# Optimization experiments

Measured on AMD Instinct MI355X. Metric: run time of the kernel, lower is better.

Reference implementation:

```python
import jax, jax.numpy as jnp
import numpy as np

B, S, E = 2, 2048, 1024
H, D = 16, 64  # num_heads, head_dim


def setup_inputs() -> dict:
    key = jax.random.key(0)
    k1, k2, k3 = jax.random.split(key, 3)
    x = jax.random.normal(k1, (B, S, E), dtype=jnp.float32)
    # nnx normal() init has stddev 0.01; scale to keep magnitudes realistic
    w_qkv = jax.random.normal(k2, (E, H, 3 * D), dtype=jnp.float32) * 0.01
    w_out = jax.random.normal(k3, (H, D, E), dtype=jnp.float32) * 0.01
    return {"x": x, "w_qkv": w_qkv, "w_out": w_out}


def _attention(q, k, v):
    # q,k,v: [B, S, H, D]
    dtype = q.dtype
    logits = jnp.einsum('bqhd,bkhd->bhqk', q.astype(jnp.float32), k.astype(jnp.float32))
    logits = logits / jnp.sqrt(jnp.float32(q.shape[-1]))
    mask = jnp.tril(jnp.ones((q.shape[1], q.shape[1]), dtype=jnp.bool_))
    neg = jnp.asarray(-0.7 * jnp.finfo(logits.dtype).max, dtype=logits.dtype)
    logits = jnp.where(mask, logits, neg)
    probs = jax.nn.softmax(logits, axis=-1).astype(dtype)
    return jnp.einsum('bhqk,bkhd->bqhd', probs, v)


def reference(x, w_qkv, w_out):
    # qkv projection: [B,S,E] x [E,H,3D] -> [B,S,H,3D]
    qkv = jnp.einsum('bse,ehd->bshd', x, w_qkv)
    q, k, v = jnp.split(qkv, 3, axis=-1)
    out = _attention(q, k, v)  # [B,S,H,D]
    # output projection contracts (H,D) -> E
    return jnp.einsum('bshd,hde->bse', out, w_out)
```

## Files before the change

kernel.cpp:

```cpp
#include <hip/hip_runtime.h>

typedef unsigned short u16;
typedef unsigned int u32;
typedef __attribute__((ext_vector_type(8))) short bf16x8;
typedef __attribute__((ext_vector_type(4))) float f32x4;
typedef __attribute__((ext_vector_type(16))) float f32x16;
typedef __attribute__((ext_vector_type(4))) u32 u32x4;

#define MFMA16(a, b, c) __builtin_amdgcn_mfma_f32_16x16x32_bf16((a), (b), (c), 0, 0, 0)
#define MFMA32(a, b, c) __builtin_amdgcn_mfma_f32_32x32x16_bf16((a), (b), (c), 0, 0, 0)

__device__ __forceinline__ void async_lds16(void* lds, const void* g) {
  __builtin_amdgcn_global_load_lds(
      (const __attribute__((address_space(1))) void*)g,
      (__attribute__((address_space(3))) void*)lds, 16, 0, 0);
}

__device__ __forceinline__ u16 f2bf(float f) {
  union { float f; unsigned u; } v; v.f = f;
  unsigned r = v.u + 0x7fffu + ((v.u >> 16) & 1u);
  return (u16)(r >> 16);
}

__device__ __forceinline__ u32 cvt_pk_bf16(float lo, float hi) {
  u32 r;
  asm("v_cvt_pk_bf16_f32 %0, %1, %2" : "=v"(r) : "v"(lo), "v"(hi));
  return r;
}

__device__ __forceinline__ float exp2_fast(float x) {
  float r;
  asm("v_exp_f32 %0, %1" : "=v"(r) : "v"(x));
  return r;
}

__device__ __forceinline__ void pswap(u32& a, u32& b) {
  asm("v_permlane32_swap_b32 %0, %1" : "+v"(a), "+v"(b));
}


__device__ __forceinline__ void transpose_cvt_body(const float* __restrict__ in, u16* __restrict__ out,
                                                   int R, int C, int bx, int by,
                                                   float (*tile)[33]) {
  int c0 = bx * 32, r0 = by * 32;
  int tx = threadIdx.x & 31, ty = threadIdx.x >> 5;
#pragma unroll
  for (int i = 0; i < 32; i += 8)
    tile[ty + i][tx] = in[(long)(r0 + ty + i) * C + c0 + tx];
  __syncthreads();
#pragma unroll
  for (int i = 0; i < 32; i += 8)
    out[(long)(c0 + ty + i) * R + r0 + tx] = f2bf(tile[tx][ty + i]);
}

__global__ __launch_bounds__(256) void k_prep(const float* __restrict__ x, u16* __restrict__ xb,
                                              const float* __restrict__ w_qkv, u16* __restrict__ wqkvT,
                                              const float* __restrict__ w_out, u16* __restrict__ woutT) {
  __shared__ float tile[32][33];
  const int B = blockIdx.x;
  if (B < 4096) {
    int i = (B * 256 + threadIdx.x) * 4;
    float4 v = *(const float4*)(x + i);
    ushort4 o;
    o.x = f2bf(v.x); o.y = f2bf(v.y); o.z = f2bf(v.z); o.w = f2bf(v.w);
    *(ushort4*)(xb + i) = o;
  } else if (B < 7168) {
    int bb = B - 4096;
    transpose_cvt_body(w_qkv, wqkvT, 1024, 3072, bb % 96, bb / 96, tile);
  } else {
    int bb = B - 7168;
    transpose_cvt_body(w_out, woutT, 1024, 1024, bb & 31, bb >> 5, tile);
  }
}

__global__ __launch_bounds__(256) void k_transpose_v(const u16* __restrict__ V, u16* __restrict__ Vt) {
  int bh = blockIdx.z;
  int s0 = blockIdx.x * 32, d0 = blockIdx.y * 32;
  __shared__ u16 tile[32][33];
  int tx = threadIdx.x & 31, ty = threadIdx.x >> 5;
  const u16* Vb = V + (long)bh * 2048 * 64;
  u16* Vtb = Vt + (long)bh * 64 * 2048;
#pragma unroll
  for (int i = 0; i < 32; i += 8)
    tile[ty + i][tx] = Vb[(long)(s0 + ty + i) * 64 + d0 + tx];
  __syncthreads();
#pragma unroll
  for (int i = 0; i < 32; i += 8)
    Vtb[(long)(d0 + ty + i) * 2048 + s0 + tx] = tile[tx][ty + i];
}


template <int BM, int BN, int NW, int WN, int WCS, int MR, int NR, int NLD>
__device__ __forceinline__ void gemm_core_pipe(const u16* __restrict__ A, const u16* __restrict__ Bt,
                                               int K, long row0, long col0,
                                               u16* sA, u16* sB, f32x4 (&acc)[MR][NR]) {
  const int NTHR = NW * 64;
  const int ABYTES = BM * 64 * 2;
  const int BBYTES = BN * 64 * 2;
  const int t = threadIdx.x;
  const int lane = t & 63, g = lane >> 4, m16 = lane & 15;
  const int wid = t >> 6, wr = wid / WN, wc = wid % WN;
  const int nkt = K >> 6;

  auto stage = [&](int buf, int kt) {
    const int k0 = kt << 6;
#pragma unroll
    for (int it = 0; it < ABYTES / (NTHR * 16); ++it) {
      int i = it * NTHR + t;
      int r = i >> 3, c = i & 7, cs = c ^ (r & 7);
      async_lds16((char*)sA + buf * ABYTES + i * 16, A + (row0 + r) * K + k0 + cs * 8);
    }
#pragma unroll
    for (int it = 0; it < BBYTES / (NTHR * 16); ++it) {
      int i = it * NTHR + t;
      int r = i >> 3, c = i & 7, cs = c ^ (r & 7);
      async_lds16((char*)sB + buf * BBYTES + i * 16, Bt + (col0 + r) * K + k0 + cs * 8);
    }
  };

  stage(0, 0);
  stage(1, 1);
  int cur = 0;
  for (int kt = 0; kt < nkt; ++kt) {
    if (kt + 1 < nkt) {
      if constexpr (NLD == 7) asm volatile("s_waitcnt vmcnt(7)" ::: "memory");
      else                    asm volatile("s_waitcnt vmcnt(8)" ::: "memory");
    } else {
      asm volatile("s_waitcnt vmcnt(0)" ::: "memory");
    }
    __builtin_amdgcn_s_barrier();
    __builtin_amdgcn_sched_barrier(0);
    const char* bA = (const char*)sA + cur * ABYTES;
    const char* bB = (const char*)sB + cur * BBYTES;
#pragma unroll
    for (int kk6 = 0; kk6 < 2; ++kk6) {
      const int ke = kk6 * 32 + 8 * g;
      bf16x8 av[MR], bv[NR];
#pragma unroll
      for (int mi = 0; mi < MR; ++mi) {
        int row = wr * (MR * 16) + mi * 16 + m16;
        av[mi] = *(const bf16x8*)(bA + (row << 7) + ((ke << 1) ^ ((row & 7) << 4)));
      }
#pragma unroll
      for (int ni = 0; ni < NR; ++ni) {
        int row = wc * WCS + ni * 16 + m16;
        bv[ni] = *(const bf16x8*)(bB + (row << 7) + ((ke << 1) ^ ((row & 7) << 4)));
      }
#pragma unroll
      for (int mi = 0; mi < MR; ++mi)
#pragma unroll
        for (int ni = 0; ni < NR; ++ni)
          acc[mi][ni] = MFMA16(av[mi], bv[ni], acc[mi][ni]);
    }
    __builtin_amdgcn_sched_barrier(0);
    __builtin_amdgcn_s_barrier();
    if (kt + 2 < nkt) stage(cur, kt + 2);
    cur ^= 1;
  }
}

__global__ __launch_bounds__(512, 2) void k_gemm_qkv(const u16* __restrict__ xb, const u16* __restrict__ wT,
                                                     u16* __restrict__ Qo, u16* __restrict__ Ko,
                                                     u16* __restrict__ Vo) {
  __shared__ __align__(16) u16 sA[2 * 256 * 64];
  __shared__ __align__(16) u16 sB[2 * 192 * 64];
  f32x4 acc[8][3];
  const f32x4 z = {0.f, 0.f, 0.f, 0.f};
#pragma unroll
  for (int mi = 0; mi < 8; ++mi)
#pragma unroll
    for (int ni = 0; ni < 3; ++ni) acc[mi][ni] = z;
  const int L = blockIdx.x;
  const int xcd = L & 7, idx = L >> 3;
  const int rowt = xcd * 2 + (idx & 1);
  const int colt = idx >> 1;
  long row0 = (long)rowt * 256, col0 = (long)colt * 192;
  gemm_core_pipe<256, 192, 8, 4, 48, 8, 3, 7>(xb, wT, 1024, row0, col0, sA, sB, acc);
  const int t = threadIdx.x;
  const int lane = t & 63, g = lane >> 4, m16 = lane & 15;
  const int wid = t >> 6, wr = wid >> 2, wc = wid & 3;
  const int h = colt;
#pragma unroll
  for (int mi = 0; mi < 8; ++mi) {
#pragma unroll
    for (int ni = 0; ni < 3; ++ni) {
      int rem = wc * 48 + ni * 16 + m16;
      int which = rem >> 6, d = rem & 63;
#pragma unroll
      for (int r = 0; r < 4; ++r) {
        int row = (int)row0 + wr * 128 + mi * 16 + 4 * g + r;
        int b = row >> 11, s = row & 2047;
        long off = (((long)(b * 16 + h)) * 2048 + s) * 64 + d;
        float v = acc[mi][ni][r];
        if (which == 0) Qo[off] = f2bf(v * 0.18033688f);
        else if (which == 1) Ko[off] = f2bf(v);
        else Vo[off] = f2bf(v);
      }
    }
  }
}

__global__ __launch_bounds__(256) void k_gemm_out(const u16* __restrict__ Ob, const u16* __restrict__ wT,
                                                  float* __restrict__ out) {
  __shared__ __align__(16) u16 sA[2 * 128 * 64];
  __shared__ __align__(16) u16 sB[2 * 128 * 64];
  f32x4 acc[4][4];
  const f32x4 z = {0.f, 0.f, 0.f, 0.f};
#pragma unroll
  for (int mi = 0; mi < 4; ++mi)
#pragma unroll
    for (int ni = 0; ni < 4; ++ni) acc[mi][ni] = z;
  const int L = blockIdx.x;
  const int xcd = L & 7, idx = L >> 3;
  const int rowt = xcd * 4 + (idx & 3);
  const int colt = idx >> 2;
  long row0 = (long)rowt * 128, col0 = (long)colt * 128;
  gemm_core_pipe<128, 128, 4, 2, 64, 4, 4, 8>(Ob, wT, 1024, row0, col0, sA, sB, acc);
  const int t = threadIdx.x;
  const int lane = t & 63, g = lane >> 4, m16 = lane & 15;
  const int wid = t >> 6, wr = wid >> 1, wc = wid & 1;
#pragma unroll
  for (int mi = 0; mi < 4; ++mi) {
#pragma unroll
    for (int ni = 0; ni < 4; ++ni) {
#pragma unroll
      for (int r = 0; r < 4; ++r) {
        long row = row0 + wr * 64 + mi * 16 + 4 * g + r;
        long col = col0 + wc * 64 + ni * 16 + m16;
        out[row * 1024 + col] = acc[mi][ni][r];
      }
    }
  }
}


template <bool DIAG>
__device__ __forceinline__ void attn_sub(const char* Kt, const char* Vt, int bsub,
                                         bf16x8 qf0, bf16x8 qf1, bf16x8 qf2, bf16x8 qf3,
                                         f32x16& acc0, f32x16& acc1, float& l,
                                         int q5, int hi) {
  const int x7 = q5 & 7;
  const int rowK = (bsub * 32 + q5) << 7;
  bf16x8 k0 = *(const bf16x8*)(Kt + rowK + (((0 + hi) ^ x7) << 4));
  bf16x8 k1 = *(const bf16x8*)(Kt + rowK + (((2 + hi) ^ x7) << 4));
  bf16x8 k2 = *(const bf16x8*)(Kt + rowK + (((4 + hi) ^ x7) << 4));
  bf16x8 k3 = *(const bf16x8*)(Kt + rowK + (((6 + hi) ^ x7) << 4));
  const int rowV0 = q5 << 7, rowV1 = (q5 + 32) << 7;
  bf16x8 v00 = *(const bf16x8*)(Vt + rowV0 + (((bsub * 4 + 0 + hi) ^ x7) << 4));
  bf16x8 v01 = *(const bf16x8*)(Vt + rowV1 + (((bsub * 4 + 0 + hi) ^ x7) << 4));
  bf16x8 v10 = *(const bf16x8*)(Vt + rowV0 + (((bsub * 4 + 2 + hi) ^ x7) << 4));
  bf16x8 v11 = *(const bf16x8*)(Vt + rowV1 + (((bsub * 4 + 2 + hi) ^ x7) << 4));

  f32x16 s;
#pragma unroll
  for (int r = 0; r < 16; ++r) s[r] = 0.f;
  __builtin_amdgcn_s_setprio(1);
  s = MFMA32(k0, qf0, s);
  s = MFMA32(k1, qf1, s);
  s = MFMA32(k2, qf2, s);
  s = MFMA32(k3, qf3, s);
  __builtin_amdgcn_s_setprio(0);

  float p[16];
#pragma unroll
  for (int r = 0; r < 16; ++r) {
    float pv = exp2_fast(s[r]);
    if (DIAG) {
      int crow = (r & 3) + 8 * (r >> 2) + 4 * hi;
      pv = (crow <= q5) ? pv : 0.f;
    }
    p[r] = pv;
  }
  l += (((p[0] + p[1]) + (p[2] + p[3])) + ((p[4] + p[5]) + (p[6] + p[7]))) +
       (((p[8] + p[9]) + (p[10] + p[11])) + ((p[12] + p[13]) + (p[14] + p[15])));

  u32 a0 = cvt_pk_bf16(p[0], p[1]), a1 = cvt_pk_bf16(p[2], p[3]);
  u32 b0 = cvt_pk_bf16(p[4], p[5]), b1 = cvt_pk_bf16(p[6], p[7]);
  pswap(a0, b0); pswap(a1, b1);
  u32 c0 = cvt_pk_bf16(p[8], p[9]), c1 = cvt_pk_bf16(p[10], p[11]);
  u32 d0 = cvt_pk_bf16(p[12], p[13]), d1 = cvt_pk_bf16(p[14], p[15]);
  pswap(c0, d0); pswap(c1, d1);
  u32x4 t0; t0[0] = a0; t0[1] = a1; t0[2] = b0; t0[3] = b1;
  u32x4 t1; t1[0] = c0; t1[1] = c1; t1[2] = d0; t1[3] = d1;
  bf16x8 pa0 = __builtin_bit_cast(bf16x8, t0);
  bf16x8 pa1 = __builtin_bit_cast(bf16x8, t1);

  __builtin_amdgcn_s_setprio(1);
  acc0 = MFMA32(pa0, v00, acc0);
  acc1 = MFMA32(pa0, v01, acc1);
  acc0 = MFMA32(pa1, v10, acc0);
  acc1 = MFMA32(pa1, v11, acc1);
  __builtin_amdgcn_s_setprio(0);
}

__global__ __launch_bounds__(256) void k_attn(const u16* __restrict__ Qg, const u16* __restrict__ Kg,
                                              const u16* __restrict__ Vtg, u16* __restrict__ Og) {
  __shared__ __align__(16) u16 sK[4][64 * 64];
  __shared__ __align__(16) u16 sV[4][64 * 64];
  const int t = threadIdx.x;
  const int lane = t & 63, q5 = lane & 31, hi = lane >> 5, w = t >> 6;
  const int L = blockIdx.x;
  const int bh = L & 31, pr = L >> 5;
  const int qtA = pr, qtB = 15 - pr;
  const int b = bh >> 4, h = bh & 15;
  const u16* Qh = Qg + (long)bh * 131072;
  const u16* Kh = Kg + (long)bh * 131072;
  const u16* Vh = Vtg + (long)bh * 131072;
  char* sKb = (char*)sK;
  char* sVb = (char*)sV;

  const int sL_ = qtA * 4 + w, sH_ = qtB * 4 + w;
  const int q0L = sL_ * 32, q0H = sH_ * 32;
  const int nkt = 2 * qtB + 2;

  const u16* QpL = Qh + (long)(q0L + q5) * 64 + hi * 8;
  bf16x8 qfL0 = *(const bf16x8*)(QpL);
  bf16x8 qfL1 = *(const bf16x8*)(QpL + 16);
  bf16x8 qfL2 = *(const bf16x8*)(QpL + 32);
  bf16x8 qfL3 = *(const bf16x8*)(QpL + 48);
  const u16* QpH = Qh + (long)(q0H + q5) * 64 + hi * 8;
  bf16x8 qfH0 = *(const bf16x8*)(QpH);
  bf16x8 qfH1 = *(const bf16x8*)(QpH + 16);
  bf16x8 qfH2 = *(const bf16x8*)(QpH + 32);
  bf16x8 qfH3 = *(const bf16x8*)(QpH + 48);

  f32x16 aL0, aL1, aH0, aH1;
#pragma unroll
  for (int r = 0; r < 16; ++r) { aL0[r] = 0.f; aL1[r] = 0.f; aH0[r] = 0.f; aH1[r] = 0.f; }
  float lL = 0.f, lH = 0.f;

  auto stage = [&](int buf, int kt) {
    const int kbase = kt << 6;
#pragma unroll
    for (int ps = 0; ps < 2; ++ps) {
      int i = ps * 256 + t;
      int r = i >> 3, c = i & 7, cs = c ^ (r & 7);
      async_lds16(sKb + buf * 8192 + i * 16, Kh + (long)(kbase + r) * 64 + cs * 8);
    }
#pragma unroll
    for (int ps = 0; ps < 2; ++ps) {
      int i = ps * 256 + t;
      int d = i >> 3, c = i & 7, cs = c ^ (d & 7);
      async_lds16(sVb + buf * 8192 + i * 16, Vh + (long)d * 2048 + kbase + cs * 8);
    }
  };

  stage(0, 0);
  stage(1, 1);
  stage(2, 2);
  stage(3, 3);
#pragma unroll 1
  for (int kt = 0; kt < nkt; ++kt) {
    const int rem = nkt - kt;
    if (rem > 3)       asm volatile("s_waitcnt vmcnt(12)" ::: "memory");
    else if (rem == 3) asm volatile("s_waitcnt vmcnt(8)" ::: "memory");
    else if (rem == 2) asm volatile("s_waitcnt vmcnt(4)" ::: "memory");
    else               asm volatile("s_waitcnt vmcnt(0)" ::: "memory");
    __builtin_amdgcn_s_barrier();
    __builtin_amdgcn_sched_barrier(0);
    const char* Kt = sKb + (kt & 3) * 8192;
    const char* Vt = sVb + (kt & 3) * 8192;
    const int c2 = 2 * kt;
    if (c2 <= sH_) {
      if (c2 == sH_) attn_sub<true>(Kt, Vt, 0, qfH0, qfH1, qfH2, qfH3, aH0, aH1, lH, q5, hi);
      else           attn_sub<false>(Kt, Vt, 0, qfH0, qfH1, qfH2, qfH3, aH0, aH1, lH, q5, hi);
    }
    if (c2 + 1 <= sH_) {
      if (c2 + 1 == sH_) attn_sub<true>(Kt, Vt, 1, qfH0, qfH1, qfH2, qfH3, aH0, aH1, lH, q5, hi);
      else               attn_sub<false>(Kt, Vt, 1, qfH0, qfH1, qfH2, qfH3, aH0, aH1, lH, q5, hi);
    }
    if (c2 <= sL_) {
      if (c2 == sL_) attn_sub<true>(Kt, Vt, 0, qfL0, qfL1, qfL2, qfL3, aL0, aL1, lL, q5, hi);
      else           attn_sub<false>(Kt, Vt, 0, qfL0, qfL1, qfL2, qfL3, aL0, aL1, lL, q5, hi);
    }
    if (c2 + 1 <= sL_) {
      if (c2 + 1 == sL_) attn_sub<true>(Kt, Vt, 1, qfL0, qfL1, qfL2, qfL3, aL0, aL1, lL, q5, hi);
      else               attn_sub<false>(Kt, Vt, 1, qfL0, qfL1, qfL2, qfL3, aL0, aL1, lL, q5, hi);
    }
    __builtin_amdgcn_sched_barrier(0);
    __builtin_amdgcn_s_barrier();
    if (kt + 4 < nkt) stage(kt & 3, kt + 4);
  }

  const long orow_base = (long)b * 2048;
  lH += __shfl_xor(lH, 32);
  float liH = 1.0f / lH;
#pragma unroll
  for (int r = 0; r < 16; ++r) {
    int crow = (r & 3) + 8 * (r >> 2) + 4 * hi;
    float lf = __shfl(liH, crow);
    long orow = orow_base + q0H + crow;
    Og[orow * 1024 + h * 64 + q5] = f2bf(aH0[r] * lf);
    Og[orow * 1024 + h * 64 + 32 + q5] = f2bf(aH1[r] * lf);
  }
  lL += __shfl_xor(lL, 32);
  float liL = 1.0f / lL;
#pragma unroll
  for (int r = 0; r < 16; ++r) {
    int crow = (r & 3) + 8 * (r >> 2) + 4 * hi;
    float lf = __shfl(liL, crow);
    long orow = orow_base + q0L + crow;
    Og[orow * 1024 + h * 64 + q5] = f2bf(aL0[r] * lf);
    Og[orow * 1024 + h * 64 + 32 + q5] = f2bf(aL1[r] * lf);
  }
}


extern "C" void kernel_launch(void* const* d_in, const int* in_sizes, int n_in,
                              void* d_out, int out_size, void* d_ws, size_t ws_size,
                              hipStream_t stream) {
  const float* x = (const float*)d_in[0];
  const float* w_qkv = (const float*)d_in[1];
  const float* w_out = (const float*)d_in[2];
  float* out = (float*)d_out;
  char* ws = (char*)d_ws;

  u16* xb    = (u16*)(ws + 0);
  u16* wqkvT = (u16*)(ws + 8388608L);
  u16* woutT = (u16*)(ws + 14680064L);
  u16* Qb    = (u16*)(ws + 16777216L);
  u16* Kb    = (u16*)(ws + 25165824L);
  u16* Vb    = (u16*)(ws + 33554432L);
  u16* Vt    = (u16*)(ws + 41943040L);
  u16* Ob    = xb;

  k_prep<<<dim3(8192), 256, 0, stream>>>(x, xb, w_qkv, wqkvT, w_out, woutT);
  k_gemm_qkv<<<dim3(256), 512, 0, stream>>>(xb, wqkvT, Qb, Kb, Vb);
  k_transpose_v<<<dim3(64, 2, 32), 256, 0, stream>>>(Vb, Vt);
  k_attn<<<dim3(256), 256, 0, stream>>>(Qb, Kb, Vt, Ob);
  k_gemm_out<<<dim3(256), 256, 0, stream>>>(Ob, woutT, out);
}
```

Baseline: 113.1 us.

## Split attention accumulators by sub-block and drop second barrier with 3-deep prefetch

Each wave now keeps two independent accumulator sets, one per 32-key sub-block, so the two sub-block MFMA chains no longer depend on each other. The sets are summed only in the epilogue. The staging pipeline moves from four tiles in flight to three, issued right after the top-of-loop barrier, which removes the second per-iteration barrier. The s_setprio hints around the MFMAs are also removed. The cost is more accumulator registers and therefore lower occupancy, plus one less tile of prefetch depth.

```diff
diff --git a/kernel.cpp b/kernel.cpp
--- a/kernel.cpp
+++ b/kernel.cpp
@@ -254,12 +254,10 @@
   f32x16 s;
 #pragma unroll
   for (int r = 0; r < 16; ++r) s[r] = 0.f;
-  __builtin_amdgcn_s_setprio(1);
   s = MFMA32(k0, qf0, s);
   s = MFMA32(k1, qf1, s);
   s = MFMA32(k2, qf2, s);
   s = MFMA32(k3, qf3, s);
-  __builtin_amdgcn_s_setprio(0);
 
   float p[16];
 #pragma unroll
@@ -285,12 +283,10 @@
   bf16x8 pa0 = __builtin_bit_cast(bf16x8, t0);
   bf16x8 pa1 = __builtin_bit_cast(bf16x8, t1);
 
-  __builtin_amdgcn_s_setprio(1);
   acc0 = MFMA32(pa0, v00, acc0);
   acc1 = MFMA32(pa0, v01, acc1);
   acc0 = MFMA32(pa1, v10, acc0);
   acc1 = MFMA32(pa1, v11, acc1);
-  __builtin_amdgcn_s_setprio(0);
 }
 
 __global__ __launch_bounds__(256) void k_attn(const u16* __restrict__ Qg, const u16* __restrict__ Kg,
@@ -324,10 +320,13 @@
   bf16x8 qfH2 = *(const bf16x8*)(QpH + 32);
   bf16x8 qfH3 = *(const bf16x8*)(QpH + 48);
 
-  f32x16 aL0, aL1, aH0, aH1;
-#pragma unroll
-  for (int r = 0; r < 16; ++r) { aL0[r] = 0.f; aL1[r] = 0.f; aH0[r] = 0.f; aH1[r] = 0.f; }
-  float lL = 0.f, lH = 0.f;
+  f32x16 aL0[2], aL1[2], aH0[2], aH1[2];
+#pragma unroll
+  for (int r = 0; r < 16; ++r) {
+    aL0[0][r] = 0.f; aL1[0][r] = 0.f; aH0[0][r] = 0.f; aH1[0][r] = 0.f;
+    aL0[1][r] = 0.f; aL1[1][r] = 0.f; aH0[1][r] = 0.f; aH1[1][r] = 0.f;
+  }
+  float lL[2] = {0.f, 0.f}, lH[2] = {0.f, 0.f};
 
   auto stage = [&](int buf, int kt) {
     const int kbase = kt << 6;
@@ -348,60 +347,62 @@
   stage(0, 0);
   stage(1, 1);
   stage(2, 2);
-  stage(3, 3);
 #pragma unroll 1
   for (int kt = 0; kt < nkt; ++kt) {
     const int rem = nkt - kt;
-    if (rem > 3)       asm volatile("s_waitcnt vmcnt(12)" ::: "memory");
-    else if (rem == 3) asm volatile("s_waitcnt vmcnt(8)" ::: "memory");
+    if (rem >= 3)      asm volatile("s_waitcnt vmcnt(8)" ::: "memory");
     else if (rem == 2) asm volatile("s_waitcnt vmcnt(4)" ::: "memory");
     else               asm volatile("s_waitcnt vmcnt(0)" ::: "memory");
     __builtin_amdgcn_s_barrier();
     __builtin_amdgcn_sched_barrier(0);
+    if (kt + 3 < nkt) stage((kt + 3) & 3, kt + 3);
     const char* Kt = sKb + (kt & 3) * 8192;
     const char* Vt = sVb + (kt & 3) * 8192;
     const int c2 = 2 * kt;
     if (c2 <= sH_) {
-      if (c2 == sH_) attn_sub<true>(Kt, Vt, 0, qfH0, qfH1, qfH2, qfH3, aH0, aH1, lH, q5, hi);
-      else           attn_sub<false>(Kt, Vt, 0, qfH0, qfH1, qfH2, qfH3, aH0, aH1, lH, q5, hi);
+      if (c2 == sH_) attn_sub<true>(Kt, Vt, 0, qfH0, qfH1, qfH2, qfH3, aH0[0], aH1[0], lH[0], q5, hi);
+      else           attn_sub<false>(Kt, Vt, 0, qfH0, qfH1, qfH2, qfH3, aH0[0], aH1[0], lH[0], q5, hi);
     }
     if (c2 + 1 <= sH_) {
-      if (c2 + 1 == sH_) attn_sub<true>(Kt, Vt, 1, qfH0, qfH1, qfH2, qfH3, aH0, aH1, lH, q5, hi);
-      else               attn_sub<false>(Kt, Vt, 1, qfH0, qfH1, qfH2, qfH3, aH0, aH1, lH, q5, hi);
+      if (c2 + 1 == sH_) attn_sub<true>(Kt, Vt, 1, qfH0, qfH1, qfH2, qfH3, aH0[1], aH1[1], lH[1], q5, hi);
+      else               attn_sub<false>(Kt, Vt, 1, qfH0, qfH1, qfH2, qfH3, aH0[1], aH1[1], lH[1], q5, hi);
     }
     if (c2 <= sL_) {
-      if (c2 == sL_) attn_sub<true>(Kt, Vt, 0, qfL0, qfL1, qfL2, qfL3, aL0, aL1, lL, q5, hi);
-      else           attn_sub<false>(Kt, Vt, 0, qfL0, qfL1, qfL2, qfL3, aL0, aL1, lL, q5, hi);
+      if (c2 == sL_) attn_sub<true>(Kt, Vt, 0, qfL0, qfL1, qfL2, qfL3, aL0[0], aL1[0], lL[0], q5, hi);
+      else           attn_sub<false>(Kt, Vt, 0, qfL0, qfL1, qfL2, qfL3, aL0[0], aL1[0], lL[0], q5, hi);
     }
     if (c2 + 1 <= sL_) {
-      if (c2 + 1 == sL_) attn_sub<true>(Kt, Vt, 1, qfL0, qfL1, qfL2, qfL3, aL0, aL1, lL, q5, hi);
-      else               attn_sub<false>(Kt, Vt, 1, qfL0, qfL1, qfL2, qfL3, aL0, aL1, lL, q5, hi);
-    }
-    __builtin_amdgcn_sched_barrier(0);
-    __builtin_amdgcn_s_barrier();
-    if (kt + 4 < nkt) stage(kt & 3, kt + 4);
+      if (c2 + 1 == sL_) attn_sub<true>(Kt, Vt, 1, qfL0, qfL1, qfL2, qfL3, aL0[1], aL1[1], lL[1], q5, hi);
+      else               attn_sub<false>(Kt, Vt, 1, qfL0, qfL1, qfL2, qfL3, aL0[1], aL1[1], lL[1], q5, hi);
+    }
   }
 
   const long orow_base = (long)b * 2048;
-  lH += __shfl_xor(lH, 32);
-  float liH = 1.0f / lH;
-#pragma unroll
-  for (int r = 0; r < 16; ++r) {
-    int crow = (r & 3) + 8 * (r >> 2) + 4 * hi;
-    float lf = __shfl(liH, crow);
-    long orow = orow_base + q0H + crow;
-    Og[orow * 1024 + h * 64 + q5] = f2bf(aH0[r] * lf);
-    Og[orow * 1024 + h * 64 + 32 + q5] = f2bf(aH1[r] * lf);
-  }
-  lL += __shfl_xor(lL, 32);
-  float liL = 1.0f / lL;
-#pragma unroll
-  for (int r = 0; r < 16; ++r) {
-    int crow = (r & 3) + 8 * (r >> 2) + 4 * hi;
-    float lf = __shfl(liL, crow);
-    long orow = orow_base + q0L + crow;
-    Og[orow * 1024 + h * 64 + q5] = f2bf(aL0[r] * lf);
-    Og[orow * 1024 + h * 64 + 32 + q5] = f2bf(aL1[r] * lf);
+  {
+    float lsum = lH[0] + lH[1];
+    lsum += __shfl_xor(lsum, 32);
+    float li = 1.0f / lsum;
+#pragma unroll
+    for (int r = 0; r < 16; ++r) {
+      int crow = (r & 3) + 8 * (r >> 2) + 4 * hi;
+      float lf = __shfl(li, crow);
+      long orow = orow_base + q0H + crow;
+      Og[orow * 1024 + h * 64 + q5] = f2bf((aH0[0][r] + aH0[1][r]) * lf);
+      Og[orow * 1024 + h * 64 + 32 + q5] = f2bf((aH1[0][r] + aH1[1][r]) * lf);
+    }
+  }
+  {
+    float lsum = lL[0] + lL[1];
+    lsum += __shfl_xor(lsum, 32);
+    float li = 1.0f / lsum;
+#pragma unroll
+    for (int r = 0; r < 16; ++r) {
+      int crow = (r & 3) + 8 * (r >> 2) + 4 * hi;
+      float lf = __shfl(li, crow);
+      long orow = orow_base + q0L + crow;
+      Og[orow * 1024 + h * 64 + q5] = f2bf((aL0[0][r] + aL0[1][r]) * lf);
+      Og[orow * 1024 + h * 64 + 32 + q5] = f2bf((aL1[0][r] + aL1[1][r]) * lf);
+    }
   }
 }
 
```

After: 125.7 us. 1.11x slower.
